# Optimization experiments

Hardware: AMD Instinct MI355X
Metric: run time of the kernel (lower is better)

Reference implementation:

```python
import jax, jax.numpy as jnp
import numpy as np

N_NODES = 50000
N_EDGES = 800000
NODE_DIM = 128
EDGE_DIM = 16
OUT_DIM = 64
HEADS = 4


def setup_inputs() -> dict:
    key = jax.random.key(0)
    ks = jax.random.split(key, 12)
    x = jax.random.normal(ks[0], (N_NODES, NODE_DIM), jnp.float32)
    edge_index = jax.random.randint(ks[1], (2, N_EDGES), 0, N_NODES)
    batch = jnp.zeros((N_NODES,), jnp.int32)
    edge_attr = jax.random.normal(ks[2], (N_EDGES, EDGE_DIM), jnp.float32)
    s = 1.0 / np.sqrt(NODE_DIM)
    W = jax.random.normal(ks[3], (NODE_DIM, HEADS * OUT_DIM), jnp.float32) * s
    att_src = jax.random.normal(ks[4], (HEADS, OUT_DIM), jnp.float32) * 0.1
    att_dst = jax.random.normal(ks[5], (HEADS, OUT_DIM), jnp.float32) * 0.1
    W_e = jax.random.normal(ks[6], (EDGE_DIM, HEADS * OUT_DIM), jnp.float32) * (1.0 / np.sqrt(EDGE_DIM))
    att_edge = jax.random.normal(ks[7], (HEADS, OUT_DIM), jnp.float32) * 0.1
    bias = jnp.zeros((OUT_DIM,), jnp.float32)
    gamma = jnp.ones((OUT_DIM,), jnp.float32)
    beta = jnp.zeros((OUT_DIM,), jnp.float32)
    return {"x": x, "edge_index": edge_index, "batch": batch, "edge_attr": edge_attr,
            "W": W, "att_src": att_src, "att_dst": att_dst, "W_e": W_e,
            "att_edge": att_edge, "bias": bias, "gamma": gamma, "beta": beta}


def reference(x, edge_index, batch, edge_attr, W, att_src, att_dst, W_e, att_edge, bias, gamma, beta):
    N = x.shape[0]
    H, C = att_src.shape
    src, dst = edge_index[0], edge_index[1]
    E = src.shape[0]

    # add self loops; self-loop edge_attr = per-node mean of incoming edge attrs (PyG fill_value='mean')
    cnt = jax.ops.segment_sum(jnp.ones((E, 1), x.dtype), dst, num_segments=N)
    loop_attr = jax.ops.segment_sum(edge_attr, dst, num_segments=N) / jnp.maximum(cnt, 1.0)
    loop_idx = jnp.arange(N, dtype=src.dtype)
    src_f = jnp.concatenate([src, loop_idx])
    dst_f = jnp.concatenate([dst, loop_idx])
    ea = jnp.concatenate([edge_attr, loop_attr], axis=0)

    h = (x @ W).reshape(N, H, C)                       # [N,H,C]
    a_src = jnp.einsum('nhc,hc->nh', h, att_src)       # [N,H]
    a_dst = jnp.einsum('nhc,hc->nh', h, att_dst)
    e_emb = (ea @ W_e).reshape(-1, H, C)               # [E',H,C]
    a_edge = jnp.einsum('ehc,hc->eh', e_emb, att_edge)

    alpha = jax.nn.leaky_relu(a_src[src_f] + a_dst[dst_f] + a_edge, 0.2)  # [E',H]
    amax = jax.ops.segment_max(alpha, dst_f, num_segments=N)
    expa = jnp.exp(alpha - amax[dst_f])
    denom = jax.ops.segment_sum(expa, dst_f, num_segments=N)
    att = expa / (denom[dst_f] + 1e-16)                # segment softmax over dst

    msg = h[src_f] * att[:, :, None]                   # [E',H,C]
    out = jax.ops.segment_sum(msg, dst_f, num_segments=N)  # [N,H,C]
    out = out.mean(axis=1) + bias                      # concat=False -> head mean

    mu = out.mean(-1, keepdims=True)
    var = out.var(-1, keepdims=True)
    out = (out - mu) / jnp.sqrt(var + 1e-5) * gamma + beta
    return jax.nn.elu(out)
```

## Files before the change

kernel.cpp:

```cpp
#include <hip/hip_runtime.h>

typedef unsigned int u32;
typedef unsigned short u16;

static constexpr int NN  = 50000;
static constexpr int EE  = 800000;
static constexpr int CAP = 64;

typedef __attribute__((ext_vector_type(8))) short bf16x8;
typedef __attribute__((ext_vector_type(4))) float f32x4;
typedef __attribute__((ext_vector_type(4))) u32   u32x4;

__device__ inline float u2f(u32 u){ union{u32 i; float f;} v; v.i=u; return v.f; }
__device__ inline float bf2f(u16 u){ return u2f(((u32)u)<<16); }
__device__ inline u16 f2bf(float f){ union{float f; u32 i;} v; v.f=f; u32 i=v.i;
    return (u16)((i + 0x7fffu + ((i>>16)&1u))>>16); }
__device__ inline u32 pk2(float a, float b){ return (u32)f2bf(a) | ((u32)f2bf(b)<<16); }
__device__ inline float lrelu(float x){ return x > 0.f ? x : 0.2f*x; }

__device__ inline u32 pkh(float a, float b){
    union{ _Float16 h[2]; u32 u; } v;
    v.h[0] = (_Float16)a; v.h[1] = (_Float16)b;
    return v.u;
}
__device__ inline float hlo(u32 u){ union{u32 u; _Float16 h[2];} v; v.u=u; return (float)v.h[0]; }
__device__ inline float hhi(u32 u){ union{u32 u; _Float16 h[2];} v; v.u=u; return (float)v.h[1]; }

__device__ inline float ld(const void* base, size_t i, int f32m){
    return f32m ? ((const float*)base)[i] : bf2f(((const u16*)base)[i]);
}

__device__ inline float wsum(float v){
    #pragma unroll
    for (int m=1;m<64;m<<=1) v += __shfl_xor(v, m, 64);
    return v;
}

#if defined(__has_builtin)
#if __has_builtin(__builtin_amdgcn_fdot2_f32_bf16)
#define HAS_DOT2 1
#endif
#endif

#ifdef HAS_DOT2
typedef __attribute__((ext_vector_type(2))) __bf16 bf16x2;
#endif

__device__ inline float dot2acc(u32 hv, u32 wv, float acc){
#ifdef HAS_DOT2
    union { u32 u; bf16x2 v; } a, b; a.u = hv; b.u = wv;
    return __builtin_amdgcn_fdot2_f32_bf16(a.v, b.v, acc, false);
#else
    acc = fmaf(u2f(hv<<16),         u2f(wv<<16),         acc);
    acc = fmaf(u2f(hv&0xffff0000u), u2f(wv&0xffff0000u), acc);
    return acc;
#endif
}

__device__ inline int detect_f32(const u16* xraw){
    int lane = threadIdx.x & 63;
    bool bad = false;
    #pragma unroll
    for (int i = 0; i < 8; ++i){
        float v = bf2f(xraw[2*(lane + i*64)]);
        if (!(fabsf(v) < 1e10f)) bad = true;
    }
    return __any(bad) ? 1 : 0;
}

__device__ inline void edge_logits(const void* ea, int e, int f32m,
                                   const float* __restrict__ Ml, float* A){
    float v[16];
    if (f32m){
        const f32x4* r = ((const f32x4*)ea) + (size_t)e*4;
        f32x4 a = __builtin_nontemporal_load(r);
        f32x4 b = __builtin_nontemporal_load(r+1);
        f32x4 c = __builtin_nontemporal_load(r+2);
        f32x4 d = __builtin_nontemporal_load(r+3);
        v[0]=a[0]; v[1]=a[1]; v[2]=a[2]; v[3]=a[3];
        v[4]=b[0]; v[5]=b[1]; v[6]=b[2]; v[7]=b[3];
        v[8]=c[0]; v[9]=c[1]; v[10]=c[2]; v[11]=c[3];
        v[12]=d[0]; v[13]=d[1]; v[14]=d[2]; v[15]=d[3];
    } else {
        const u32x4* r = ((const u32x4*)ea) + (size_t)e*2;
        u32x4 q0 = __builtin_nontemporal_load(r);
        u32x4 q1 = __builtin_nontemporal_load(r+1);
        v[0]=u2f(q0[0]<<16); v[1]=u2f(q0[0]&0xffff0000u);
        v[2]=u2f(q0[1]<<16); v[3]=u2f(q0[1]&0xffff0000u);
        v[4]=u2f(q0[2]<<16); v[5]=u2f(q0[2]&0xffff0000u);
        v[6]=u2f(q0[3]<<16); v[7]=u2f(q0[3]&0xffff0000u);
        v[8]=u2f(q1[0]<<16); v[9]=u2f(q1[0]&0xffff0000u);
        v[10]=u2f(q1[1]<<16); v[11]=u2f(q1[1]&0xffff0000u);
        v[12]=u2f(q1[2]<<16); v[13]=u2f(q1[2]&0xffff0000u);
        v[14]=u2f(q1[3]<<16); v[15]=u2f(q1[3]&0xffff0000u);
    }
    float a0=0,a1=0,a2=0,a3=0;
    #pragma unroll
    for (int j = 0; j < 16; ++j){
        a0 = fmaf(v[j], Ml[j*4+0], a0);
        a1 = fmaf(v[j], Ml[j*4+1], a1);
        a2 = fmaf(v[j], Ml[j*4+2], a2);
        a3 = fmaf(v[j], Ml[j*4+3], a3);
    }
    A[0]=a0; A[1]=a1; A[2]=a2; A[3]=a3;
}

__global__ __launch_bounds__(256) void k_prep(const u16* __restrict__ xraw,
                                              const void* __restrict__ W,
                                              const void* __restrict__ att_src,
                                              const void* __restrict__ att_dst,
                                              const void* __restrict__ W_e,
                                              const void* __restrict__ att_edge,
                                              int* __restrict__ flag,
                                              u16* __restrict__ Wt,
                                              float* __restrict__ Mv,
                                              int* __restrict__ deg){
    int f32m = detect_f32(xraw);
    int b = blockIdx.x, t = threadIdx.x;
    if (b == 0){
        if (t == 0) *flag = f32m;
        if (t < 64){
            int d = t >> 2, h = t & 3;
            float s = 0.f;
            for (int c = 0; c < 64; ++c)
                s += ld(W_e, d*256 + h*64 + c, f32m) * ld(att_edge, h*64 + c, f32m);
            Mv[t] = s;
        }
    } else if (b <= 128){
        int i = (b-1)*256 + t;
        int k = i >> 8, j = i & 255;
        int n = (j & 3)*64 + (j >> 2);
        Wt[j*128 + k] = f2bf(ld(W, (size_t)k*256 + n, f32m));
    } else if (b <= 136){
        int i = (b-129)*256 + t;
        int c = i >> 7, k = i & 127;
        float s = 0.f;
        if (c < 8){
            int h = c & 3;
            const void* att = (c < 4) ? att_src : att_dst;
            for (int j = 0; j < 64; ++j)
                s += ld(W, (size_t)k*256 + h*64 + j, f32m) * ld(att, h*64 + j, f32m);
        }
        Wt[(size_t)(256 + c)*128 + k] = f2bf(s);
    } else {
        int i = (b-137)*256 + t;
        if (i < NN) deg[i] = 0;
    }
}

__global__ __launch_bounds__(256) void k_gx(const void* __restrict__ x,
                                            const u16* __restrict__ Wt,
                                            const int* __restrict__ flag,
                                            u16* __restrict__ hbuf,
                                            float* __restrict__ a_src,
                                            float* __restrict__ a_dst,
                                            const int* __restrict__ ei,
                                            const void* __restrict__ ea,
                                            const float* __restrict__ Mv,
                                            int* __restrict__ deg,
                                            uint4* __restrict__ brec,
                                            int N, int E, int GB){
    int t = threadIdx.x;
    int f32m = *flag;
    if ((int)blockIdx.x < GB){
        int row0 = blockIdx.x*64;
        int wave = t >> 6, lane = t & 63;
        int l15 = lane & 15, quad = lane >> 4;
        int grow = row0 + wave*16 + l15; if (grow >= N) grow = N-1;
        bf16x8 afr[4];
        if (f32m){
            const f32x4* xf = (const f32x4*)x;
            #pragma unroll
            for (int s=0;s<4;++s){
                f32x4 v0 = __builtin_nontemporal_load(&xf[(size_t)grow*32 + s*8 + quad*2]);
                f32x4 v1 = __builtin_nontemporal_load(&xf[(size_t)grow*32 + s*8 + quad*2 + 1]);
                union{ u32x4 u; bf16x8 b; } cv;
                cv.u[0] = pk2(v0[0],v0[1]); cv.u[1] = pk2(v0[2],v0[3]);
                cv.u[2] = pk2(v1[0],v1[1]); cv.u[3] = pk2(v1[2],v1[3]);
                afr[s] = cv.b;
            }
        } else {
            const u16* x16 = (const u16*)x;
            #pragma unroll
            for (int s=0;s<4;++s)
                afr[s] = __builtin_nontemporal_load(
                    (const bf16x8*)&x16[(size_t)grow*128 + s*32 + quad*8]);
        }
        f32x4 acc[17];
        #pragma unroll
        for (int tl=0;tl<17;++tl){
            f32x4 a = {0.f,0.f,0.f,0.f};
            #pragma unroll
            for (int s=0;s<4;++s){
                bf16x8 bfr = *(const bf16x8*)&Wt[(size_t)(tl*16 + l15)*128 + s*32 + quad*8];
                a = __builtin_amdgcn_mfma_f32_16x16x32_bf16(afr[s], bfr, a, 0, 0, 0);
            }
            acc[tl] = a;
        }
        int rbase = row0 + wave*16 + quad*4;
        #pragma unroll
        for (int r=0;r<4;++r){
            int gr = rbase + r;
            if (gr < N){
                if (l15 < 4)      a_src[gr*4 + l15]     = acc[16][r];
                else if (l15 < 8) a_dst[gr*4 + (l15-4)] = acc[16][r];
            }
        }
        #pragma unroll
        for (int r=0;r<4;++r){
            int gr = rbase + r;
            if (gr < N){
                #pragma unroll
                for (int tl=0;tl<16;++tl)
                    hbuf[(size_t)gr*256 + tl*16 + l15] = f2bf(acc[tl][r]);
            }
        }
    } else {
        int e = ((int)blockIdx.x - GB)*256 + t;
        if (e < E){
            int src = __builtin_nontemporal_load(&ei[e]);
            int dst = __builtin_nontemporal_load(&ei[E + e]);
            int slot = atomicAdd(&deg[dst], 1);
            float A[4];
            edge_logits(ea, e, f32m, Mv, A);
            if (slot < CAP)
                brec[(size_t)dst*CAP + slot] =
                    make_uint4((u32)src, pkh(A[0], A[1]), pkh(A[2], A[3]), 0u);
        }
    }
}

__global__ __launch_bounds__(256) void k_node(const int* __restrict__ deg,
                                              const uint4* __restrict__ brec,
                                              const float* __restrict__ a_src,
                                              const float* __restrict__ a_dst,
                                              const u16* __restrict__ hbuf,
                                              const void* __restrict__ bias,
                                              const void* __restrict__ gamma,
                                              const void* __restrict__ beta,
                                              const int* __restrict__ flag,
                                              void* __restrict__ out, int N){
    __shared__ uint4 lrec[4][CAP+4];
    int f32m = *flag;
    int lane = threadIdx.x & 63;
    int slot = threadIdx.x >> 6;
    int n = blockIdx.x*4 + slot;
    int dg = deg[n];
    int dc = dg < CAP ? dg : CAP;
    float4 an  = ((const float4*)a_src)[n];
    float4 adn = ((const float4*)a_dst)[n];
    bool v0 = lane < dc;
    u32 src = (u32)n;
    float w0=0.f,w1=0.f,w2=0.f,w3=0.f;
    float a0=0.f,a1=0.f,a2=0.f,a3=0.f;
    if (v0){
        const u32x4* rp = (const u32x4*)brec + ((size_t)n*CAP + lane);
        u32x4 r = __builtin_nontemporal_load(rp);
        src = r[0];
        a0 = hlo(r[1]); a1 = hhi(r[1]); a2 = hlo(r[2]); a3 = hhi(r[2]);
        float4 asg = ((const float4*)a_src)[src];
        w0 = expf(lrelu(asg.x + adn.x + a0));
        w1 = expf(lrelu(asg.y + adn.y + a1));
        w2 = expf(lrelu(asg.z + adn.z + a2));
        w3 = expf(lrelu(asg.w + adn.w + a3));
    }
    float dn0 = wsum(w0), dn1 = wsum(w1), dn2 = wsum(w2), dn3 = wsum(w3);
    float invd = 1.f / (float)(dg > 1 ? dg : 1);
    float ge0 = wsum(a0)*invd, ge1 = wsum(a1)*invd;
    float ge2 = wsum(a2)*invd, ge3 = wsum(a3)*invd;
    float exS0 = expf(lrelu(an.x + adn.x + ge0));
    float exS1 = expf(lrelu(an.y + adn.y + ge1));
    float exS2 = expf(lrelu(an.z + adn.z + ge2));
    float exS3 = expf(lrelu(an.w + adn.w + ge3));
    float i0 = 0.25f/(dn0 + exS0 + 1e-16f);
    float i1 = 0.25f/(dn1 + exS1 + 1e-16f);
    float i2 = 0.25f/(dn2 + exS2 + 1e-16f);
    float i3 = 0.25f/(dn3 + exS3 + 1e-16f);
    if (v0)
        lrec[slot][lane] = make_uint4(src, pk2(w0*i0, w1*i1), pk2(w2*i2, w3*i3), 0u);
    if (lane == 0)
        lrec[slot][dc] = make_uint4((u32)n, pk2(exS0*i0, exS1*i1), pk2(exS2*i2, exS3*i3), 0u);
    else if (lane <= 3)
        lrec[slot][dc + lane] = make_uint4((u32)n, 0u, 0u, 0u);
    __syncthreads();
    int T = dc + 1;
    int iters = (T + 3) >> 2;
    int half = lane >> 5, l5 = lane & 31;
    const uint4* hb4 = (const uint4*)hbuf;
    float acc0 = 0.f, acc1 = 0.f;
    uint4 rA0 = lrec[slot][half];
    uint4 rA1 = lrec[slot][2 + half];
    uint4 hA0 = hb4[(size_t)rA0.x*32 + l5];
    uint4 hA1 = hb4[(size_t)rA1.x*32 + l5];
    uint4 rB0, rB1, hB0, hB1;
    if (iters > 1){
        rB0 = lrec[slot][4 + half];
        rB1 = lrec[slot][6 + half];
        hB0 = hb4[(size_t)rB0.x*32 + l5];
        hB1 = hb4[(size_t)rB1.x*32 + l5];
    }
    int i = 0;
    while (true){
        {
            bool pf = (i + 2 < iters);
            uint4 nr0, nr1, nh0, nh1;
            if (pf){
                nr0 = lrec[slot][4*(i+2) + half];
                nr1 = lrec[slot][4*(i+2) + 2 + half];
                nh0 = hb4[(size_t)nr0.x*32 + l5];
                nh1 = hb4[(size_t)nr1.x*32 + l5];
            }
            acc0 = dot2acc(hA0.x, rA0.y, acc0);
            acc0 = dot2acc(hA0.y, rA0.z, acc0);
            acc1 = dot2acc(hA0.z, rA0.y, acc1);
            acc1 = dot2acc(hA0.w, rA0.z, acc1);
            acc0 = dot2acc(hA1.x, rA1.y, acc0);
            acc0 = dot2acc(hA1.y, rA1.z, acc0);
            acc1 = dot2acc(hA1.z, rA1.y, acc1);
            acc1 = dot2acc(hA1.w, rA1.z, acc1);
            if (pf){ rA0=nr0; rA1=nr1; hA0=nh0; hA1=nh1; }
            if (++i >= iters) break;
        }
        {
            bool pf = (i + 2 < iters);
            uint4 nr0, nr1, nh0, nh1;
            if (pf){
                nr0 = lrec[slot][4*(i+2) + half];
                nr1 = lrec[slot][4*(i+2) + 2 + half];
                nh0 = hb4[(size_t)nr0.x*32 + l5];
                nh1 = hb4[(size_t)nr1.x*32 + l5];
            }
            acc0 = dot2acc(hB0.x, rB0.y, acc0);
            acc0 = dot2acc(hB0.y, rB0.z, acc0);
            acc1 = dot2acc(hB0.z, rB0.y, acc1);
            acc1 = dot2acc(hB0.w, rB0.z, acc1);
            acc0 = dot2acc(hB1.x, rB1.y, acc0);
            acc0 = dot2acc(hB1.y, rB1.z, acc0);
            acc1 = dot2acc(hB1.z, rB1.y, acc1);
            acc1 = dot2acc(hB1.w, rB1.z, acc1);
            if (pf){ rB0=nr0; rB1=nr1; hB0=nh0; hB1=nh1; }
            if (++i >= iters) break;
        }
    }
    acc0 += __shfl_xor(acc0, 32, 64);
    acc1 += __shfl_xor(acc1, 32, 64);
    float va = __shfl(acc0, lane>>1, 64);
    float vb = __shfl(acc1, lane>>1, 64);
    float o = ((lane & 1) ? vb : va) + ld(bias, lane, f32m);
    float mu = wsum(o) * (1.f/64.f);
    float d = o - mu;
    float var = wsum(d*d) * (1.f/64.f);
    float y = d * rsqrtf(var + 1e-5f) * ld(gamma, lane, f32m) + ld(beta, lane, f32m);
    y = y > 0.f ? y : expf(y) - 1.f;
    if (f32m) __builtin_nontemporal_store(y, &((float*)out)[(size_t)n*64 + lane]);
    else      __builtin_nontemporal_store(f2bf(y), &((u16*)out)[(size_t)n*64 + lane]);
}

extern "C" void kernel_launch(void* const* d_in, const int* in_sizes, int n_in,
                              void* d_out, int out_size, void* d_ws, size_t ws_size,
                              hipStream_t stream){
    const void* x        = d_in[0];
    const int*  ei       = (const int*)d_in[1];
    const void* ea       = d_in[3];
    const void* W        = d_in[4];
    const void* att_src  = d_in[5];
    const void* att_dst  = d_in[6];
    const void* W_e      = d_in[7];
    const void* att_edge = d_in[8];
    const void* bias     = d_in[9];
    const void* gamma    = d_in[10];
    const void* beta     = d_in[11];
    const int N = NN, E = EE;

    char* p = (char*)d_ws;
    auto alloc = [&](size_t bytes){ void* r = (void*)p; p += (bytes + 255) & ~(size_t)255; return r; };
    int*   deg   = (int*)  alloc((size_t)N*4);
    float* Mv    = (float*)alloc(64*4);
    float* a_src = (float*)alloc((size_t)N*16);
    float* a_dst = (float*)alloc((size_t)N*16);
    uint4* brec  = (uint4*)alloc((size_t)N*CAP*16);
    u16*   hbuf  = (u16*)  alloc((size_t)N*256*2);
    u16*   Wt    = (u16*)  alloc((size_t)272*128*2);
    int*   flag  = (int*)  alloc(256);

    const int GB = (N + 63)/64;
    const int EB = (E + 255)/256;
    const int PB = 137 + (N + 255)/256;

    k_prep<<<PB, 256, 0, stream>>>((const u16*)x, W, att_src, att_dst, W_e, att_edge,
                                   flag, Wt, Mv, deg);
    k_gx<<<GB + EB, 256, 0, stream>>>(x, Wt, flag, hbuf, a_src, a_dst,
                                      ei, ea, Mv, deg, brec, N, E, GB);
    k_node<<<N/4, 256, 0, stream>>>(deg, brec, a_src, a_dst, hbuf,
                                    bias, gamma, beta, flag, d_out, N);
}
```

Measured before the change: 275.0 us.

## Write edge records contiguously and bucket only edge indices per destination

Edge records are now written coalesced to a per-edge array, and each destination bucket holds only a 4-byte edge index instead of a scattered 16-byte record. Edge blocks each handle two edges and are interleaved with GEMM blocks so both kinds of work run together, and the GEMM outputs use nontemporal stores. The goal is to cut scattered-write traffic in the scatter phase. The cost is an extra dependent indirect load in the node kernel.

```diff
diff --git a/kernel.cpp b/kernel.cpp
--- a/kernel.cpp
+++ b/kernel.cpp
@@ -158,12 +158,17 @@
                                             const void* __restrict__ ea,
                                             const float* __restrict__ Mv,
                                             int* __restrict__ deg,
-                                            uint4* __restrict__ brec,
+                                            u32x4* __restrict__ erec,
+                                            u32* __restrict__ bidx,
                                             int N, int E, int GB){
     int t = threadIdx.x;
     int f32m = *flag;
-    if ((int)blockIdx.x < GB){
-        int row0 = blockIdx.x*64;
+    int b = (int)blockIdx.x;
+    bool isg; int wid;
+    if (b < 2*GB){ isg = !(b & 1); wid = b >> 1; }
+    else         { isg = false;    wid = b - GB; }
+    if (isg){
+        int row0 = wid*64;
         int wave = t >> 6, lane = t & 63;
         int l15 = lane & 15, quad = lane >> 4;
         int grow = row0 + wave*16 + l15; if (grow >= N) grow = N-1;
@@ -202,8 +207,10 @@
         for (int r=0;r<4;++r){
             int gr = rbase + r;
             if (gr < N){
-                if (l15 < 4)      a_src[gr*4 + l15]     = acc[16][r];
-                else if (l15 < 8) a_dst[gr*4 + (l15-4)] = acc[16][r];
+                if (l15 < 4)
+                    __builtin_nontemporal_store(acc[16][r], &a_src[gr*4 + l15]);
+                else if (l15 < 8)
+                    __builtin_nontemporal_store(acc[16][r], &a_dst[gr*4 + (l15-4)]);
             }
         }
         #pragma unroll
@@ -212,26 +219,34 @@
             if (gr < N){
                 #pragma unroll
                 for (int tl=0;tl<16;++tl)
-                    hbuf[(size_t)gr*256 + tl*16 + l15] = f2bf(acc[tl][r]);
+                    __builtin_nontemporal_store(f2bf(acc[tl][r]),
+                        &hbuf[(size_t)gr*256 + tl*16 + l15]);
             }
         }
     } else {
-        int e = ((int)blockIdx.x - GB)*256 + t;
-        if (e < E){
+        int base = wid*512 + t;
+        #pragma unroll
+        for (int j=0;j<2;++j){
+            int e = base + j*256;
+            if (e >= E) continue;
             int src = __builtin_nontemporal_load(&ei[e]);
             int dst = __builtin_nontemporal_load(&ei[E + e]);
             int slot = atomicAdd(&deg[dst], 1);
             float A[4];
             edge_logits(ea, e, f32m, Mv, A);
+            u32x4 rec;
+            rec[0] = (u32)src; rec[1] = pkh(A[0],A[1]);
+            rec[2] = pkh(A[2],A[3]); rec[3] = 0u;
+            __builtin_nontemporal_store(rec, &erec[e]);
             if (slot < CAP)
-                brec[(size_t)dst*CAP + slot] =
-                    make_uint4((u32)src, pkh(A[0], A[1]), pkh(A[2], A[3]), 0u);
+                bidx[(size_t)dst*CAP + slot] = (u32)e;
         }
     }
 }
 
 __global__ __launch_bounds__(256) void k_node(const int* __restrict__ deg,
-                                              const uint4* __restrict__ brec,
+                                              const u32* __restrict__ bidx,
+                                              const u32x4* __restrict__ erec,
                                               const float* __restrict__ a_src,
                                               const float* __restrict__ a_dst,
                                               const u16* __restrict__ hbuf,
@@ -254,8 +269,8 @@
     float w0=0.f,w1=0.f,w2=0.f,w3=0.f;
     float a0=0.f,a1=0.f,a2=0.f,a3=0.f;
     if (v0){
-        const u32x4* rp = (const u32x4*)brec + ((size_t)n*CAP + lane);
-        u32x4 r = __builtin_nontemporal_load(rp);
+        u32 e = __builtin_nontemporal_load(&bidx[(size_t)n*CAP + lane]);
+        u32x4 r = __builtin_nontemporal_load(&erec[e]);
         src = r[0];
         a0 = hlo(r[1]); a1 = hhi(r[1]); a2 = hlo(r[2]); a3 = hhi(r[2]);
         float4 asg = ((const float4*)a_src)[src];
@@ -378,19 +393,20 @@
     float* Mv    = (float*)alloc(64*4);
     float* a_src = (float*)alloc((size_t)N*16);
     float* a_dst = (float*)alloc((size_t)N*16);
-    uint4* brec  = (uint4*)alloc((size_t)N*CAP*16);
+    u32x4* erec  = (u32x4*)alloc((size_t)E*16);
+    u32*   bidx  = (u32*)  alloc((size_t)N*CAP*4);
     u16*   hbuf  = (u16*)  alloc((size_t)N*256*2);
     u16*   Wt    = (u16*)  alloc((size_t)272*128*2);
     int*   flag  = (int*)  alloc(256);
 
     const int GB = (N + 63)/64;
-    const int EB = (E + 255)/256;
+    const int EB = (E + 511)/512;
     const int PB = 137 + (N + 255)/256;
 
     k_prep<<<PB, 256, 0, stream>>>((const u16*)x, W, att_src, att_dst, W_e, att_edge,
                                    flag, Wt, Mv, deg);
     k_gx<<<GB + EB, 256, 0, stream>>>(x, Wt, flag, hbuf, a_src, a_dst,
-                                      ei, ea, Mv, deg, brec, N, E, GB);
-    k_node<<<N/4, 256, 0, stream>>>(deg, brec, a_src, a_dst, hbuf,
+                                      ei, ea, Mv, deg, erec, bidx, N, E, GB);
+    k_node<<<N/4, 256, 0, stream>>>(deg, bidx, erec, a_src, a_dst, hbuf,
                                     bias, gamma, beta, flag, d_out, N);
 }
```

Result: slower. 296.6 us (+7.8%).
